# Optimization experiments

Measured on AMD Instinct MI355X. Metric: run time of the kernel, lower is better.

## Reference

```python
import jax, jax.numpy as jnp
import numpy as np

H = 2048   # hidden_dim
NH = 16    # num_heads
NG = 4     # num_groups
WS = 256   # window_size
SS = 128   # shift_size
B, N = 2, 4096
C = H // NG          # per-group channel dim = 512
HD = C // NH         # windowed head dim = 32


def setup_inputs() -> dict:
    key = jax.random.key(0)
    ks = jax.random.split(key, 10)
    s = 1.0 / np.sqrt(H)
    return {
        "inputs": jax.random.normal(ks[0], (B, N, H), jnp.float32),
        "context": jax.random.normal(ks[1], (B, N, H), jnp.float32),
        "mask": jnp.ones((1,), jnp.bool_),
        "Wq": jax.random.normal(ks[2], (H, H // NH), jnp.float32) * s,
        "bq": jnp.zeros((H // NH,), jnp.float32),
        "Wk": jax.random.normal(ks[3], (H, H // (NH * NG)), jnp.float32) * s,
        "bk": jnp.zeros((H // (NH * NG),), jnp.float32),
        "Wv": jax.random.normal(ks[4], (H, H // (NH * NG)), jnp.float32) * s,
        "bv": jnp.zeros((H // (NH * NG),), jnp.float32),
        "Wo": jax.random.normal(ks[5], (H, H), jnp.float32) * s,
        "bo": jnp.zeros((H,), jnp.float32),
    }


def _rotate_half(x):
    x1, x2 = jnp.split(x, 2, axis=-1)
    return jnp.concatenate((-x2, x1), axis=-1)


def reference(inputs, context, mask, Wq, bq, Wk, bk, Wv, bv, Wo, bo):
    Bq, Nq, _ = inputs.shape
    q = inputs @ Wq + bq                 # (B, N, H/NH)
    k = context @ Wk + bk                # (B, N, H/(NH*NG))
    v = context @ Wv + bv

    # group queries, element-wise repeat channels (faithful to jnp.repeat axis=-1)
    gq = q.reshape(Bq, Nq, NG, -1)
    gq = jnp.repeat(gq, NH, axis=-1).transpose(2, 0, 1, 3)   # (G, B, N, C)
    k = jnp.repeat(k, NH, axis=-1)                            # (B, N, C)
    v = jnp.repeat(v, NH, axis=-1)

    # RoPE tables for dim C = H // NG
    inv_freq = 1.0 / (10000.0 ** (jnp.arange(0, C, 2, dtype=jnp.float32) / C))
    t = jnp.arange(Nq, dtype=jnp.float32)
    freqs = jnp.outer(t, inv_freq)
    emb = jnp.concatenate((freqs, freqs), axis=-1)            # (N, C)
    cos, sin = jnp.cos(emb), jnp.sin(emb)

    def apply_rope(x):  # (B, N, C)
        return x * cos + _rotate_half(x) * sin

    k_r = apply_rope(k)
    causal = jnp.tril(jnp.ones((WS, WS), jnp.float32))        # multiplicative mask (faithful)
    scale = jnp.sqrt(jnp.float32(C))                           # dim_key = C in source

    def wpart(x):  # (B, N, C) -> (nW, B, WS, C)
        return x.reshape(Bq, -1, WS, C).transpose(1, 0, 2, 3)

    def process_group(qg):  # qg: (B, N, C)
        qg = apply_rope(qg)
        qw, kw, vw = wpart(qg), wpart(k_r), wpart(v)
        nW = qw.shape[0]
        # faithful raw reshape head split (no transpose), as in source
        qh = qw.reshape(nW, Bq, NH, WS, HD)
        kh = kw.reshape(nW, Bq, NH, WS, HD)
        vh = vw.reshape(nW, Bq, NH, WS, HD)
        scores = jnp.einsum('wbhid,wbhjd->wbhij', qh, kh) / scale
        scores = scores * causal
        attn = jax.nn.softmax(scores, axis=-1)
        av = jnp.einsum('wbhij,wbhjd->wbhid', attn, vh)
        av = av.transpose(0, 1, 3, 2, 4).reshape(nW, Bq, WS, C)
        av = jnp.roll(av, -SS, axis=1)        # roll over batch axis, faithful to source
        merged = av.transpose(1, 0, 2, 3).reshape(Bq, Nq, C)
        return merged, attn

    out_groups, attn_maps = jax.vmap(process_group)(gq)       # (G,B,N,C), (G,nW,B,h,w,w)
    cv = jnp.moveaxis(out_groups, 0, 2).reshape(Bq, Nq, H)    # == concat over groups on last axis
    out = cv @ Wo + bo
    return out, attn_maps
```

## Files before the change

### kernel.cpp

```cpp
#include <hip/hip_runtime.h>
#include <hip/hip_bf16.h>
#include <math.h>


typedef short bf16x8 __attribute__((ext_vector_type(8)));
typedef float f32x4 __attribute__((ext_vector_type(4)));
typedef unsigned short u16x8 __attribute__((ext_vector_type(8)));
typedef unsigned short u16x2 __attribute__((ext_vector_type(2)));

#define AS1 __attribute__((address_space(1)))
#define AS3 __attribute__((address_space(3)))

__device__ __forceinline__ void gload16(const void* g, void* l) {
  __builtin_amdgcn_global_load_lds((const AS1 void*)g, (AS3 void*)l, 16, 0, 0);
}

__device__ __forceinline__ unsigned short f2bf(float f) {
  unsigned u = __float_as_uint(f);
  u += 0x7FFFu + ((u >> 16) & 1u);
  return (unsigned short)(u >> 16);
}

__global__ __launch_bounds__(256) void k_prep(float* __restrict__ cosT,
                                              float* __restrict__ sinT,
                                              const float* __restrict__ Wq,
                                              const float* __restrict__ Wk,
                                              const float* __restrict__ Wv,
                                              unsigned short* __restrict__ WqT,
                                              unsigned short* __restrict__ WkvT,
                                              const float* __restrict__ Wo,
                                              unsigned short* __restrict__ WoR,
                                              const float* __restrict__ bk,
                                              const float* __restrict__ bv,
                                              float* __restrict__ biaskv) {
  __shared__ float tile[32][33];
  const int bi = blockIdx.x;
  const int tid = threadIdx.x;

  if (bi < 4096) {
    int t = bi * 256 + tid;
    int p = t >> 8, idx = t & 255;
    float invf = (float)exp2(-(double)idx * (13.287712379549449 / 256.0));
    float ang = (float)p * invf;
    float s, c;
    sincosf(ang, &s, &c);
    cosT[t] = c;
    sinT[t] = s;
    return;
  }
  if (bi < 4480) {
    const float* in;
    unsigned short* out;
    int C, rowOff, tc, tr;
    if (bi < 4352) {
      int i = bi - 4096;
      in = Wq; out = WqT; C = 128; rowOff = 0;
      tc = (i & 3) * 32; tr = (i >> 2) * 32;
    } else if (bi < 4416) {
      int i = bi - 4352;
      in = Wk; out = WkvT; C = 32; rowOff = 0;
      tc = 0; tr = i * 32;
    } else {
      int i = bi - 4416;
      in = Wv; out = WkvT; C = 32; rowOff = 32;
      tc = 0; tr = i * 32;
    }
    int lx = tid & 31, ly = tid >> 5;
#pragma unroll
    for (int s2 = 0; s2 < 4; ++s2) {
      int rr = ly + s2 * 8;
      tile[rr][lx] = in[(size_t)(tr + rr) * C + tc + lx];
    }
    __syncthreads();
#pragma unroll
    for (int s2 = 0; s2 < 4; ++s2) {
      int cc = ly + s2 * 8;
      out[(size_t)(rowOff + tc + cc) * 2048 + tr + lx] = f2bf(tile[lx][cc]);
    }
    return;
  }
  if (bi < 5504) {
    int i = bi - 4480;
    const int kk = i >> 3;
    const int c = (i & 7) * 256 + tid;
    const int base = (kk >> 5) * 512 + ((kk >> 1) & 15) * 32 + (kk & 1) * 16;
    float s = 0.f;
#pragma unroll
    for (int d = 0; d < 16; ++d) s += Wo[(size_t)(base + d) * 2048 + c];
    WoR[(size_t)c * 128 + kk] = f2bf(s);
    return;
  }
  if (tid < 128) biaskv[tid] = (tid < 32) ? bk[tid] : ((tid < 64) ? bv[tid - 32] : 0.f);
}

__global__ __launch_bounds__(256) void k_qkv(const float* __restrict__ A0,
                                             const unsigned short* __restrict__ B0,
                                             float* __restrict__ C0,
                                             const float* __restrict__ bias0,
                                             const float* __restrict__ A1,
                                             const unsigned short* __restrict__ B1,
                                             float* __restrict__ C1,
                                             const float* __restrict__ bias1,
                                             int K) {
  const float* A = blockIdx.z ? A1 : A0;
  const unsigned short* Bt = blockIdx.z ? B1 : B0;
  float* C = blockIdx.z ? C1 : C0;
  const float* bias = blockIdx.z ? bias1 : bias0;

  __shared__ unsigned short Al[2][32 * 32];
  __shared__ unsigned short Bl[2][128 * 32];
  const int tid = threadIdx.x;
  const int wave = tid >> 6, lane = tid & 63;
  const int wm = wave >> 1, wn = wave & 1;
  f32x4 acc[4] = {};
  const int lrow = lane & 15, kq = (lane >> 4) * 8;
  const size_t abase = (size_t)blockIdx.x * 32;
  const int rB = lane >> 2, cB = (lane & 3) * 8;
  const int ar = tid >> 3, ac = (tid & 7) * 4;
  const float* aptr = A + (abase + ar) * (size_t)K + ac;

#define QKV_STAGEB(buf, kt)                                                     \
  {                                                                             \
    gload16(Bt + (size_t)(wave * 16 + rB) * K + (kt) + cB,                      \
            &Bl[buf][(wave * 16) * 32]);                                        \
    gload16(Bt + (size_t)(64 + wave * 16 + rB) * K + (kt) + cB,                 \
            &Bl[buf][(64 + wave * 16) * 32]);                                   \
  }

  float4 r0 = *(const float4*)(aptr + 0);
  QKV_STAGEB(0, 0);
  *(ushort4*)&Al[0][ar * 32 + ac] =
      make_ushort4(f2bf(r0.x), f2bf(r0.y), f2bf(r0.z), f2bf(r0.w));
  __syncthreads();

  int cur = 0;
  for (int kt = 0; kt < K; kt += 32) {
    const bool more = (kt + 32) < K;
    if (more) {
      r0 = *(const float4*)(aptr + kt + 32);
      QKV_STAGEB(cur ^ 1, kt + 32);
    }
    bf16x8 af = *(const bf16x8*)&Al[cur][(wm * 16 + lrow) * 32 + kq];
    bf16x8 bg[4];
#pragma unroll
    for (int n = 0; n < 4; ++n)
      bg[n] = *(const bf16x8*)&Bl[cur][(wn * 64 + n * 16 + lrow) * 32 + kq];
#pragma unroll
    for (int n = 0; n < 4; ++n)
      acc[n] = __builtin_amdgcn_mfma_f32_16x16x32_bf16(af, bg[n], acc[n], 0, 0, 0);
    if (more)
      *(ushort4*)&Al[cur ^ 1][ar * 32 + ac] =
          make_ushort4(f2bf(r0.x), f2bf(r0.y), f2bf(r0.z), f2bf(r0.w));
    __syncthreads();
    cur ^= 1;
  }
#undef QKV_STAGEB
  const int mb = (int)abase + wm * 16;
#pragma unroll
  for (int n = 0; n < 4; ++n)
#pragma unroll
    for (int r2 = 0; r2 < 4; ++r2) {
      int row = mb + (lane >> 4) * 4 + r2;
      int col = wn * 64 + n * 16 + lrow;
      C[(size_t)row * 128 + col] = acc[n][r2] + bias[col];
    }
}

template <int BM, int BN>
__global__ __launch_bounds__(256) void k_gemm(const unsigned short* __restrict__ A,
                                              const unsigned short* __restrict__ Bt,
                                              float* __restrict__ C,
                                              const float* __restrict__ bias,
                                              int M, int N, int K) {
  __shared__ unsigned short Al[2][BM * 32];
  __shared__ unsigned short Bl[2][BN * 32];
  const int tid = threadIdx.x;
  const int wave = tid >> 6, lane = tid & 63;
  const int wm = wave >> 1, wn = wave & 1;
  constexpr int FM = BM / 32, FN = BN / 32;
  f32x4 acc[FM][FN] = {};
  const int lrow = lane & 15, kq = (lane >> 4) * 8;
  const size_t abase = (size_t)blockIdx.x * BM;
  const size_t bbase = (size_t)blockIdx.y * BN;
  const int rA = lane >> 2, cA = (lane & 3) * 8;

#define STAGE(buf, kt)                                                                \
  {                                                                                   \
    _Pragma("unroll") for (int c2 = 0; c2 < BM / 64; ++c2) {                          \
      int rr = (c2 * 4 + wave) * 16 + rA;                                             \
      gload16(A + (abase + rr) * K + (kt) + cA, &Al[buf][(c2 * 4 + wave) * 512]);     \
    }                                                                                 \
    _Pragma("unroll") for (int c2 = 0; c2 < BN / 64; ++c2) {                          \
      int rr = (c2 * 4 + wave) * 16 + rA;                                             \
      gload16(Bt + (bbase + rr) * K + (kt) + cA, &Bl[buf][(c2 * 4 + wave) * 512]);    \
    }                                                                                 \
  }

  STAGE(0, 0);
  __syncthreads();
  int cur = 0;
  for (int kt = 0; kt < K; kt += 32) {
    if (kt + 32 < K) STAGE(cur ^ 1, kt + 32);
    bf16x8 af[FM], bg[FN];
#pragma unroll
    for (int m = 0; m < FM; ++m)
      af[m] = *(const bf16x8*)&Al[cur][(wm * (BM / 2) + m * 16 + lrow) * 32 + kq];
#pragma unroll
    for (int n = 0; n < FN; ++n)
      bg[n] = *(const bf16x8*)&Bl[cur][(wn * (BN / 2) + n * 16 + lrow) * 32 + kq];
#pragma unroll
    for (int m = 0; m < FM; ++m)
#pragma unroll
      for (int n = 0; n < FN; ++n)
        acc[m][n] = __builtin_amdgcn_mfma_f32_16x16x32_bf16(af[m], bg[n], acc[m][n], 0, 0, 0);
    __syncthreads();
    cur ^= 1;
  }
#undef STAGE
  const int mb = blockIdx.x * BM + wm * (BM / 2);
  const int nb = blockIdx.y * BN + wn * (BN / 2);
#pragma unroll
  for (int m = 0; m < FM; ++m)
#pragma unroll
    for (int n = 0; n < FN; ++n)
#pragma unroll
      for (int r2 = 0; r2 < 4; ++r2) {
        int row = mb + m * 16 + (lane >> 4) * 4 + r2;
        int col = nb + n * 16 + lrow;
        float v = acc[m][n][r2] + bias[col];
        __builtin_nontemporal_store(v, &C[(size_t)row * N + col]);
      }
}

__global__ __launch_bounds__(256, 3) void k_attn(const float* __restrict__ qbuf,
                                                 const float* __restrict__ kvbuf,
                                                 const float* __restrict__ cosT,
                                                 const float* __restrict__ sinT,
                                                 float* __restrict__ attn_out,
                                                 unsigned short* __restrict__ pv_out) {
  __shared__ unsigned short Qb[256 * 32];
  __shared__ unsigned short Kb[256 * 32];
  __shared__ float stage[4][16 * 68];
  __shared__ float vpair[512];
  float (*qraw)[32] = (float (*)[32])(&stage[0][0]);
  float (*kraw)[32] = (float (*)[32])(&stage[0][0] + 512);

  const int t = threadIdx.x;
  const int unit = blockIdx.x;
  const int h = unit & 15, b = (unit >> 4) & 1, w = (unit >> 5) & 15, g = unit >> 9;
  const int row0 = b * 4096 + w * 256 + 16 * h;
  const int p0 = w * 256 + 16 * h;

  for (int e = t; e < 512; e += 256) {
    int r = e >> 5, ch = e & 31;
    size_t gi = (size_t)(row0 + r) * 128;
    qraw[r][ch] = qbuf[gi + g * 32 + ch];
    kraw[r][ch] = kvbuf[gi + ch];
    vpair[r * 32 + ch] = kvbuf[gi + 32 + ch];
  }
  __syncthreads();

  {
    const int r = t >> 4, cb = t & 15;
    const int ch = 2 * cb;
    const int po = (cb < 8) ? 16 : -16;
    const float sg = (cb < 8) ? -1.f : 1.f;
    const float4* c4 = (const float4*)(cosT + (size_t)(p0 + r) * 256 + 32 * (cb & 7));
    const float4* s4 = (const float4*)(sinT + (size_t)(p0 + r) * 256 + 32 * (cb & 7));
    float qa0 = qraw[r][ch], qa1 = qraw[r][ch + 1];
    float qp0 = qraw[r][ch + po], qp1 = qraw[r][ch + po + 1];
    float ka0 = kraw[r][ch], ka1 = kraw[r][ch + 1];
    float kp0 = kraw[r][ch + po], kp1 = kraw[r][ch + po + 1];
    const float rs = 0.044194173824159216f;
    unsigned short qs[32], ks[32];
#pragma unroll
    for (int dq = 0; dq < 8; ++dq) {
      float4 cc = c4[dq], ss = s4[dq];
      float qa = (dq < 4) ? qa0 : qa1, qp = (dq < 4) ? qp0 : qp1;
      float ka = (dq < 4) ? ka0 : ka1, kp = (dq < 4) ? kp0 : kp1;
      qs[dq * 4 + 0] = f2bf((qa * cc.x + sg * qp * ss.x) * rs);
      qs[dq * 4 + 1] = f2bf((qa * cc.y + sg * qp * ss.y) * rs);
      qs[dq * 4 + 2] = f2bf((qa * cc.z + sg * qp * ss.z) * rs);
      qs[dq * 4 + 3] = f2bf((qa * cc.w + sg * qp * ss.w) * rs);
      ks[dq * 4 + 0] = f2bf(ka * cc.x + sg * kp * ss.x);
      ks[dq * 4 + 1] = f2bf(ka * cc.y + sg * kp * ss.y);
      ks[dq * 4 + 2] = f2bf(ka * cc.z + sg * kp * ss.z);
      ks[dq * 4 + 3] = f2bf(ka * cc.w + sg * kp * ss.w);
    }
#pragma unroll
    for (int q4 = 0; q4 < 4; ++q4) {
      *(u16x8*)&Qb[t * 32 + q4 * 8] = *(u16x8*)&qs[q4 * 8];
      *(u16x8*)&Kb[t * 32 + q4 * 8] = *(u16x8*)&ks[q4 * 8];
    }
  }
  __syncthreads();

  const int wv = t >> 6, lane = t & 63;
  const int lm = lane & 15, lq = lane >> 4;
  const int kq = lq * 8;
  const size_t abase = (size_t)unit * 65536;
  float* stw = &stage[wv][0];

#pragma unroll
  for (int mt = 0; mt < 4; ++mt) {
    const int iT = wv * 4 + mt;
    const int i = iT * 16 + lm;
    bf16x8 bQ = *(const bf16x8*)&Qb[(iT * 16 + lm) * 32 + kq];
    f32x4 acc[16];
#pragma unroll
    for (int nt = 0; nt < 16; ++nt) {
      bf16x8 aK = *(const bf16x8*)&Kb[(nt * 16 + lm) * 32 + kq];
      f32x4 z = {0.f, 0.f, 0.f, 0.f};
      acc[nt] = __builtin_amdgcn_mfma_f32_16x16x32_bf16(aK, bQ, z, 0, 0, 0);
    }
    float ls = 0.f, pa = 0.f, pb = 0.f;
#pragma unroll
    for (int nt = 0; nt < 16; ++nt) {
      float4 v01 = *(const float4*)&vpair[nt * 32 + lq * 8];
      float4 v23 = *(const float4*)&vpair[nt * 32 + lq * 8 + 4];
#pragma unroll
      for (int r = 0; r < 4; ++r) {
        int j = nt * 16 + lq * 4 + r;
        float s = (j <= i) ? acc[nt][r] : 0.f;
        float e = __expf(s);
        acc[nt][r] = e;
        ls += e;
      }
      pa += acc[nt][0] * v01.x + acc[nt][1] * v01.z + acc[nt][2] * v23.x + acc[nt][3] * v23.z;
      pb += acc[nt][0] * v01.y + acc[nt][1] * v01.w + acc[nt][2] * v23.y + acc[nt][3] * v23.w;
    }
    ls += __shfl_xor(ls, 16);
    ls += __shfl_xor(ls, 32);
    pa += __shfl_xor(pa, 16);
    pa += __shfl_xor(pa, 32);
    pb += __shfl_xor(pb, 16);
    pb += __shfl_xor(pb, 32);
    const float invl = 1.f / ls;

    if (lq == 0) {
      u16x2 pvv = {f2bf(pa * invl), f2bf(pb * invl)};
      *(u16x2*)&pv_out[(size_t)(b * 4096 + w * 256 + i) * 128 + g * 32 + h * 2] = pvv;
    }

#pragma unroll
    for (int nc = 0; nc < 4; ++nc) {
#pragma unroll
      for (int nt2 = 0; nt2 < 4; ++nt2) {
        int nt = nc * 4 + nt2;
        int phys = (nt2 * 4 + lq + lm) & 15;
        f32x4 p4 = acc[nt] * invl;
        *(f32x4*)&stw[lm * 68 + phys * 4] = p4;
      }
      asm volatile("s_waitcnt lgkmcnt(0)" ::: "memory");
      __builtin_amdgcn_sched_barrier(0);
#pragma unroll
      for (int rb = 0; rb < 4; ++rb) {
        int rr = rb * 4 + lq;
        int c = lm;
        int phys = (c + rr) & 15;
        f32x4 pvv = *(const f32x4*)&stw[rr * 68 + phys * 4];
        f32x4* gp = (f32x4*)&attn_out[abase + (size_t)(iT * 16 + rr) * 256 + nc * 64 + c * 4];
        __builtin_nontemporal_store(pvv, gp);
      }
      asm volatile("s_waitcnt lgkmcnt(0)" ::: "memory");
      __builtin_amdgcn_sched_barrier(0);
    }
  }
}

extern "C" void kernel_launch(void* const* d_in, const int* in_sizes, int n_in,
                              void* d_out, int out_size, void* d_ws, size_t ws_size,
                              hipStream_t stream) {
  const float* inputs  = (const float*)d_in[0];
  const float* context = (const float*)d_in[1];
  const float* Wq = (const float*)d_in[3];
  const float* bq = (const float*)d_in[4];
  const float* Wk = (const float*)d_in[5];
  const float* bk = (const float*)d_in[6];
  const float* Wv = (const float*)d_in[7];
  const float* bv = (const float*)d_in[8];
  const float* Wo = (const float*)d_in[9];
  const float* bo = (const float*)d_in[10];
  float* out = (float*)d_out;
  float* attn_out = out + 16777216;

  char* wsb = (char*)d_ws;
  size_t o = 0;
  float* cosT = (float*)(wsb + o);            o += 4194304;
  float* sinT = (float*)(wsb + o);            o += 4194304;
  unsigned short* WqT  = (unsigned short*)(wsb + o); o += 524288;
  unsigned short* WkvT = (unsigned short*)(wsb + o); o += 524288;
  unsigned short* WoR  = (unsigned short*)(wsb + o); o += 524288;
  float* qbuf  = (float*)(wsb + o);           o += 4194304;
  float* kvbuf = (float*)(wsb + o);           o += 4194304;
  unsigned short* pv = (unsigned short*)(wsb + o); o += 2097152;
  float* biaskv = (float*)(wsb + o);          o += 512;

  k_prep<<<5505, 256, 0, stream>>>(cosT, sinT, Wq, Wk, Wv, WqT, WkvT, Wo, WoR,
                                   bk, bv, biaskv);

  k_qkv<<<dim3(256, 1, 2), 256, 0, stream>>>(
      inputs, WqT, qbuf, bq, context, WkvT, kvbuf, biaskv, 2048);

  k_attn<<<2048, 256, 0, stream>>>(qbuf, kvbuf, cosT, sinT, attn_out, pv);

  k_gemm<128, 128><<<dim3(64, 16), 256, 0, stream>>>(pv, WoR, out, bo, 8192, 2048, 128);
}
```

Before: 221.4 us.

## Move RoPE table and Wo reduction work into QKV GEMM launch as extra blocks

The RoPE cos/sin table generation and the Wo row-sum reduction move out of the serial prep kernel. They now run as extra blocks appended to the QKV projection grid, so this independent work can fill idle CUs while the 512 GEMM blocks run, and the prep kernel shrinks to the weight transposes. The RoPE path also now computes two elements per thread with float2 stores. Separately, the explicit lgkmcnt waits and sched barriers around the LDS transpose in the attention output store are removed, which relies on the compiler inserting the needed waits. Risks are that the extra blocks in k_qkv could delay GEMM blocks, and the barrier removal could change scheduling or correctness.

After: 227.9 us. +3.0%, slower.

```diff
diff --git a/kernel.cpp b/kernel.cpp
--- a/kernel.cpp
+++ b/kernel.cpp
@@ -21,15 +21,11 @@
   return (unsigned short)(u >> 16);
 }
 
-__global__ __launch_bounds__(256) void k_prep(float* __restrict__ cosT,
-                                              float* __restrict__ sinT,
-                                              const float* __restrict__ Wq,
+__global__ __launch_bounds__(256) void k_prep(const float* __restrict__ Wq,
                                               const float* __restrict__ Wk,
                                               const float* __restrict__ Wv,
                                               unsigned short* __restrict__ WqT,
                                               unsigned short* __restrict__ WkvT,
-                                              const float* __restrict__ Wo,
-                                              unsigned short* __restrict__ WoR,
                                               const float* __restrict__ bk,
                                               const float* __restrict__ bv,
                                               float* __restrict__ biaskv) {
@@ -37,31 +33,19 @@
   const int bi = blockIdx.x;
   const int tid = threadIdx.x;
 
-  if (bi < 4096) {
-    int t = bi * 256 + tid;
-    int p = t >> 8, idx = t & 255;
-    float invf = (float)exp2(-(double)idx * (13.287712379549449 / 256.0));
-    float ang = (float)p * invf;
-    float s, c;
-    sincosf(ang, &s, &c);
-    cosT[t] = c;
-    sinT[t] = s;
-    return;
-  }
-  if (bi < 4480) {
+  if (bi < 384) {
     const float* in;
     unsigned short* out;
     int C, rowOff, tc, tr;
-    if (bi < 4352) {
-      int i = bi - 4096;
+    if (bi < 256) {
       in = Wq; out = WqT; C = 128; rowOff = 0;
-      tc = (i & 3) * 32; tr = (i >> 2) * 32;
-    } else if (bi < 4416) {
-      int i = bi - 4352;
+      tc = (bi & 3) * 32; tr = (bi >> 2) * 32;
+    } else if (bi < 320) {
+      int i = bi - 256;
       in = Wk; out = WkvT; C = 32; rowOff = 0;
       tc = 0; tr = i * 32;
     } else {
-      int i = bi - 4416;
+      int i = bi - 320;
       in = Wv; out = WkvT; C = 32; rowOff = 32;
       tc = 0; tr = i * 32;
     }
@@ -77,17 +61,6 @@
       int cc = ly + s2 * 8;
       out[(size_t)(rowOff + tc + cc) * 2048 + tr + lx] = f2bf(tile[lx][cc]);
     }
-    return;
-  }
-  if (bi < 5504) {
-    int i = bi - 4480;
-    const int kk = i >> 3;
-    const int c = (i & 7) * 256 + tid;
-    const int base = (kk >> 5) * 512 + ((kk >> 1) & 15) * 32 + (kk & 1) * 16;
-    float s = 0.f;
-#pragma unroll
-    for (int d = 0; d < 16; ++d) s += Wo[(size_t)(base + d) * 2048 + c];
-    WoR[(size_t)c * 128 + kk] = f2bf(s);
     return;
   }
   if (tid < 128) biaskv[tid] = (tid < 32) ? bk[tid] : ((tid < 64) ? bv[tid - 32] : 0.f);
@@ -101,7 +74,38 @@
                                              const unsigned short* __restrict__ B1,
                                              float* __restrict__ C1,
                                              const float* __restrict__ bias1,
+                                             float* __restrict__ cosT,
+                                             float* __restrict__ sinT,
+                                             const float* __restrict__ Wo,
+                                             unsigned short* __restrict__ WoR,
                                              int K) {
+  const int tid = threadIdx.x;
+  if (blockIdx.x >= 256) {
+    if (blockIdx.z == 0) {
+      int e = (blockIdx.x - 256) * 512 + tid * 2;
+      int p = e >> 8, idx = e & 255;
+      float i0 = (float)exp2(-(double)idx * (13.287712379549449 / 256.0));
+      float i1 = (float)exp2(-(double)(idx + 1) * (13.287712379549449 / 256.0));
+      float s0, c0, s1, c1;
+      sincosf((float)p * i0, &s0, &c0);
+      sincosf((float)p * i1, &s1, &c1);
+      *(float2*)&cosT[e] = make_float2(c0, c1);
+      *(float2*)&sinT[e] = make_float2(s0, s1);
+    } else {
+      int i = blockIdx.x - 256;
+      if (i < 1024) {
+        const int kk = i >> 3;
+        const int c = (i & 7) * 256 + tid;
+        const int base = (kk >> 5) * 512 + ((kk >> 1) & 15) * 32 + (kk & 1) * 16;
+        float s = 0.f;
+#pragma unroll
+        for (int d = 0; d < 16; ++d) s += Wo[(size_t)(base + d) * 2048 + c];
+        WoR[(size_t)c * 128 + kk] = f2bf(s);
+      }
+    }
+    return;
+  }
+
   const float* A = blockIdx.z ? A1 : A0;
   const unsigned short* Bt = blockIdx.z ? B1 : B0;
   float* C = blockIdx.z ? C1 : C0;
@@ -109,7 +113,6 @@
 
   __shared__ unsigned short Al[2][32 * 32];
   __shared__ unsigned short Bl[2][128 * 32];
-  const int tid = threadIdx.x;
   const int wave = tid >> 6, lane = tid & 63;
   const int wm = wave >> 1, wn = wave & 1;
   f32x4 acc[4] = {};
@@ -351,8 +354,6 @@
         f32x4 p4 = acc[nt] * invl;
         *(f32x4*)&stw[lm * 68 + phys * 4] = p4;
       }
-      asm volatile("s_waitcnt lgkmcnt(0)" ::: "memory");
-      __builtin_amdgcn_sched_barrier(0);
 #pragma unroll
       for (int rb = 0; rb < 4; ++rb) {
         int rr = rb * 4 + lq;
@@ -362,8 +363,6 @@
         f32x4* gp = (f32x4*)&attn_out[abase + (size_t)(iT * 16 + rr) * 256 + nc * 64 + c * 4];
         __builtin_nontemporal_store(pvv, gp);
       }
-      asm volatile("s_waitcnt lgkmcnt(0)" ::: "memory");
-      __builtin_amdgcn_sched_barrier(0);
     }
   }
 }
@@ -396,11 +395,11 @@
   unsigned short* pv = (unsigned short*)(wsb + o); o += 2097152;
   float* biaskv = (float*)(wsb + o);          o += 512;
 
-  k_prep<<<5505, 256, 0, stream>>>(cosT, sinT, Wq, Wk, Wv, WqT, WkvT, Wo, WoR,
-                                   bk, bv, biaskv);
-
-  k_qkv<<<dim3(256, 1, 2), 256, 0, stream>>>(
-      inputs, WqT, qbuf, bq, context, WkvT, kvbuf, biaskv, 2048);
+  k_prep<<<385, 256, 0, stream>>>(Wq, Wk, Wv, WqT, WkvT, bk, bv, biaskv);
+
+  k_qkv<<<dim3(2304, 1, 2), 256, 0, stream>>>(
+      inputs, WqT, qbuf, bq, context, WkvT, kvbuf, biaskv,
+      cosT, sinT, Wo, WoR, 2048);
 
   k_attn<<<2048, 256, 0, stream>>>(qbuf, kvbuf, cosT, sinT, attn_out, pv);
 
```
